# Optimization experiments

Measured on AMD Instinct MI355X. Metric: run time of the kernel, lower is better.

Reference implementation:

```python
import jax, jax.numpy as jnp
import numpy as np

GROUP_SIZE = 64

def _dequant(wq, scale, zero):
    # HQQ groupwise dequant: W = (Wq - zero) * scale, groups along input dim.
    out_dim, in_dim = wq.shape
    g = in_dim // GROUP_SIZE
    w = (wq.astype(jnp.float32).reshape(out_dim, g, GROUP_SIZE) - zero[:, :, None]) * scale[:, :, None]
    return w.reshape(out_dim, in_dim)

def setup_inputs() -> dict:
    key = jax.random.key(0)
    ks = jax.random.split(key, 10)
    T, H, I = 256, 4096, 14336
    G1, G2 = H // GROUP_SIZE, I // GROUP_SIZE  # 64, 224
    x = jax.random.normal(ks[0], (T, H), dtype=jnp.float32)
    w1_q = jax.random.randint(ks[1], (I, H), 0, 16, dtype=jnp.int32)
    w1_scale = jax.random.uniform(ks[2], (I, G1), dtype=jnp.float32) * 0.02
    w1_zero = jax.random.uniform(ks[3], (I, G1), dtype=jnp.float32) * 8.0
    w3_q = jax.random.randint(ks[4], (I, H), 0, 16, dtype=jnp.int32)
    w3_scale = jax.random.uniform(ks[5], (I, G1), dtype=jnp.float32) * 0.02
    w3_zero = jax.random.uniform(ks[6], (I, G1), dtype=jnp.float32) * 8.0
    w2_q = jax.random.randint(ks[7], (H, I), 0, 16, dtype=jnp.int32)
    w2_scale = jax.random.uniform(ks[8], (H, G2), dtype=jnp.float32) * 0.02
    w2_zero = jax.random.uniform(ks[9], (H, G2), dtype=jnp.float32) * 8.0
    return {"x": x, "w1_q": w1_q, "w1_scale": w1_scale, "w1_zero": w1_zero,
            "w3_q": w3_q, "w3_scale": w3_scale, "w3_zero": w3_zero,
            "w2_q": w2_q, "w2_scale": w2_scale, "w2_zero": w2_zero}

def reference(x, w1_q, w1_scale, w1_zero, w3_q, w3_scale, w3_zero, w2_q, w2_scale, w2_zero):
    w1 = _dequant(w1_q, w1_scale, w1_zero)  # [I, H]
    w3 = _dequant(w3_q, w3_scale, w3_zero)  # [I, H]
    w2 = _dequant(w2_q, w2_scale, w2_zero)  # [H, I]
    gate = jax.nn.silu(jnp.einsum('th,ih->ti', x, w1))  # [T, I]
    up = jnp.einsum('th,ih->ti', x, w3)                 # [T, I]
    return jnp.einsum('ti,hi->th', gate * up, w2)       # [T, H]
```

## Files before the change

kernel.cpp:

```cpp
#include <hip/hip_runtime.h>
#include <cstdint>
#include <cstddef>

#define T_DIM 256
#define H_DIM 4096
#define I_DIM 14336

typedef __attribute__((ext_vector_type(8))) short s8v;
typedef __attribute__((ext_vector_type(4))) float f4v;

static constexpr size_t XS_BYTES   = (size_t)T_DIM * H_DIM * 2;
static constexpr size_t ACT_OFF    = XS_BYTES;
static constexpr size_t ACT_BYTES  = (size_t)T_DIM * I_DIM * 2;
static constexpr size_t PART_OFF   = ACT_OFF + ACT_BYTES;
static constexpr size_t PART_BYTES = 8ull * T_DIM * H_DIM * 4;
static constexpr size_t WS_NEEDED  = PART_OFF + PART_BYTES;

__device__ __forceinline__ unsigned short f2bf(float f) {
    unsigned u = __builtin_bit_cast(unsigned, f);
    u += 0x7fffu + ((u >> 16) & 1u);
    return (unsigned short)(u >> 16);
}

__device__ __forceinline__ void bar_read() {
    __builtin_amdgcn_sched_barrier(0);
    __builtin_amdgcn_s_barrier();
    __builtin_amdgcn_sched_barrier(0);
}
__device__ __forceinline__ void bar_write() {
    __builtin_amdgcn_sched_barrier(0);
    asm volatile("s_waitcnt lgkmcnt(0)" ::: "memory");
    __builtin_amdgcn_s_barrier();
    __builtin_amdgcn_sched_barrier(0);
}

__device__ __forceinline__ s8v dq8(const int4 qa, const int4 qb, float s, float ns) {
    union { unsigned short u[8]; s8v v; } r;
    r.u[0] = f2bf(fmaf((float)qa.x, s, ns));
    r.u[1] = f2bf(fmaf((float)qa.y, s, ns));
    r.u[2] = f2bf(fmaf((float)qa.z, s, ns));
    r.u[3] = f2bf(fmaf((float)qa.w, s, ns));
    r.u[4] = f2bf(fmaf((float)qb.x, s, ns));
    r.u[5] = f2bf(fmaf((float)qb.y, s, ns));
    r.u[6] = f2bf(fmaf((float)qb.z, s, ns));
    r.u[7] = f2bf(fmaf((float)qb.w, s, ns));
    return r.v;
}

__global__ __launch_bounds__(256) void k_prep(const float* __restrict__ x,
                                              unsigned short* __restrict__ xs) {
    int gs   = blockIdx.x * 256 + threadIdx.x;
    int kt   = gs >> 11;
    int rem  = gs & 2047;
    int row  = rem >> 3;
    int slot = rem & 7;
    const float* xp = x + (size_t)row * H_DIM + kt * 64 + slot * 8;
    float4 a = *(const float4*)xp;
    float4 b = *(const float4*)(xp + 4);
    union { unsigned short u[8]; s8v v; } r;
    r.u[0] = f2bf(a.x); r.u[1] = f2bf(a.y); r.u[2] = f2bf(a.z); r.u[3] = f2bf(a.w);
    r.u[4] = f2bf(b.x); r.u[5] = f2bf(b.y); r.u[6] = f2bf(b.z); r.u[7] = f2bf(b.w);
    *(s8v*)(xs + (size_t)kt * 16384 + (size_t)row * 64 + (size_t)slot * 8) = r.v;
}

struct P1 { int4 x0, x1, x2, x3, q1a, q1b, q3a, q3b; float s1, z1, s3, z3; };

__global__ __launch_bounds__(512) void k_gemm1(
    const int* __restrict__ w1q, const float* __restrict__ w1s, const float* __restrict__ w1z,
    const int* __restrict__ w3q, const float* __restrict__ w3s, const float* __restrict__ w3z,
    const unsigned short* __restrict__ xs, unsigned short* __restrict__ act)
{
    __shared__ unsigned char lds[2][49152];
    const int tid  = threadIdx.x;
    const int blk  = blockIdx.x;
    const int n0   = blk * 64;
    const int wid  = tid >> 6;
    const int lane = tid & 63;
    const int wr   = wid >> 1;
    const int wc   = wid & 1;
    const int lr   = lane & 15;
    const int lkb  = lane >> 4;
    const int aswz = (lr & 7) << 4;

    const int sr = tid >> 3, sl = tid & 7;
    const int sbyte = sr * 128 + ((sl * 16) ^ ((sr & 7) << 4));
    const int4*  xbase = (const int4*)xs;
    const size_t wrow  = (size_t)(n0 + sr) * H_DIM;
    const float* s1p = w1s + (size_t)(n0 + sr) * 64;
    const float* z1p = w1z + (size_t)(n0 + sr) * 64;
    const float* s3p = w3s + (size_t)(n0 + sr) * 64;
    const float* z3p = w3z + (size_t)(n0 + sr) * 64;

    f4v accg[4][2], accu[4][2];
    const f4v fz = {0.f, 0.f, 0.f, 0.f};
    #pragma unroll
    for (int i = 0; i < 4; ++i)
        #pragma unroll
        for (int j = 0; j < 2; ++j) { accg[i][j] = fz; accu[i][j] = fz; }

    auto load = [&](int kt, P1& p) {
        const int4* xp = xbase + kt * 2048 + sr * 8 + sl;
        p.x0 = xp[0]; p.x1 = xp[512]; p.x2 = xp[1024]; p.x3 = xp[1536];
        const int4* p1 = (const int4*)(w1q + wrow + kt * 64 + sl * 8);
        const int4* p3 = (const int4*)(w3q + wrow + kt * 64 + sl * 8);
        p.q1a = p1[0]; p.q1b = p1[1]; p.q3a = p3[0]; p.q3b = p3[1];
        p.s1 = s1p[kt]; p.z1 = z1p[kt]; p.s3 = s3p[kt]; p.z3 = z3p[kt];
    };
    auto store = [&](const P1& p, unsigned char* b) {
        *(int4*)(b + sbyte)         = p.x0;
        *(int4*)(b + sbyte + 8192)  = p.x1;
        *(int4*)(b + sbyte + 16384) = p.x2;
        *(int4*)(b + sbyte + 24576) = p.x3;
        *(s8v*)(b + 32768 + sbyte) = dq8(p.q1a, p.q1b, p.s1, -p.z1 * p.s1);
        *(s8v*)(b + 40960 + sbyte) = dq8(p.q3a, p.q3b, p.s3, -p.z3 * p.s3);
    };
    auto compute = [&](const unsigned char* b) {
        #pragma unroll
        for (int kf = 0; kf < 2; ++kf) {
            const int kb = (kf * 64 + lkb * 16) ^ aswz;
            s8v a[4];
            #pragma unroll
            for (int mf = 0; mf < 4; ++mf)
                a[mf] = *(const s8v*)(b + (wr * 64 + mf * 16 + lr) * 128 + kb);
            s8v b1[2], b3[2];
            #pragma unroll
            for (int nf = 0; nf < 2; ++nf) {
                const int rbo = (wc * 32 + nf * 16 + lr) * 128 + kb;
                b1[nf] = *(const s8v*)(b + 32768 + rbo);
                b3[nf] = *(const s8v*)(b + 40960 + rbo);
            }
            #pragma unroll
            for (int mf = 0; mf < 4; ++mf)
                #pragma unroll
                for (int nf = 0; nf < 2; ++nf) {
                    accg[mf][nf] = __builtin_amdgcn_mfma_f32_16x16x32_bf16(a[mf], b1[nf], accg[mf][nf], 0, 0, 0);
                    accu[mf][nf] = __builtin_amdgcn_mfma_f32_16x16x32_bf16(a[mf], b3[nf], accu[mf][nf], 0, 0, 0);
                }
        }
    };

    P1 A, B;
    load(0, A);
    store(A, lds[0]);
    load(1, B);
    bar_write();

    for (int it = 0; it < 32; ++it) {
        const int t = it * 2;
        load(t + 2 > 63 ? 63 : t + 2, A);
        compute(lds[0]);
        bar_read();
        store(B, lds[1]);
        bar_write();
        load(t + 3 > 63 ? 63 : t + 3, B);
        compute(lds[1]);
        bar_read();
        store(A, lds[0]);
        bar_write();
    }

    unsigned char* actb = (unsigned char*)act + (size_t)blk * 32768;
    #pragma unroll
    for (int mf = 0; mf < 4; ++mf)
        #pragma unroll
        for (int nf = 0; nf < 2; ++nf)
            #pragma unroll
            for (int r = 0; r < 4; ++r) {
                const int m  = wr * 64 + mf * 16 + lkb * 4 + r;
                const int nl = wc * 32 + nf * 16 + lr;
                float g = accg[mf][nf][r];
                float u = accu[mf][nf][r];
                float sg = g / (1.0f + __expf(-g));
                *(unsigned short*)(actb + m * 128 + nl * 2) = f2bf(sg * u);
            }
}

struct P2 { int4 a0, a1, a2, a3, q0, q1, q2, q3; float s2, z2; };

template<bool ATOMIC>
__global__ __launch_bounds__(512) void k_gemm2(
    const int* __restrict__ w2q, const float* __restrict__ w2s, const float* __restrict__ w2z,
    const unsigned short* __restrict__ act, float* __restrict__ outp)
{
    __shared__ unsigned char lds[2][49152];
    const int tid  = threadIdx.x;
    const int nb   = blockIdx.x & 31;
    const int kc   = blockIdx.x >> 5;
    const int n0   = nb * 128;
    const int wid  = tid >> 6;
    const int lane = tid & 63;
    const int wr   = wid >> 2;
    const int wc   = wid & 3;
    const int lr   = lane & 15;
    const int lkb  = lane >> 4;
    const int aswz = (lr & 7) << 4;

    const int sr = tid >> 3, sl = tid & 7;
    const int abyte = sr * 128 + ((sl * 16) ^ ((sr & 7) << 4));
    const int r2 = tid >> 2, sq = tid & 3;
    const int wb0 = r2 * 128 + (((sq * 2) * 16)     ^ ((r2 & 7) << 4));
    const int wb1 = r2 * 128 + (((sq * 2 + 1) * 16) ^ ((r2 & 7) << 4));
    const int4*  abase = (const int4*)act;
    const size_t w2row = (size_t)(n0 + r2) * I_DIM;
    const float* s2p = w2s + (size_t)(n0 + r2) * 224;
    const float* z2p = w2z + (size_t)(n0 + r2) * 224;

    f4v acc[8][2];
    const f4v fz = {0.f, 0.f, 0.f, 0.f};
    #pragma unroll
    for (int i = 0; i < 8; ++i) { acc[i][0] = fz; acc[i][1] = fz; }

    auto load = [&](int kt, P2& p) {
        const int4* ap = abase + kt * 2048 + sr * 8 + sl;
        p.a0 = ap[0]; p.a1 = ap[512]; p.a2 = ap[1024]; p.a3 = ap[1536];
        const int4* wp = (const int4*)(w2q + w2row + kt * 64 + sq * 16);
        p.q0 = wp[0]; p.q1 = wp[1]; p.q2 = wp[2]; p.q3 = wp[3];
        p.s2 = s2p[kt]; p.z2 = z2p[kt];
    };
    auto store = [&](const P2& p, unsigned char* b) {
        *(int4*)(b + abyte)         = p.a0;
        *(int4*)(b + abyte + 8192)  = p.a1;
        *(int4*)(b + abyte + 16384) = p.a2;
        *(int4*)(b + abyte + 24576) = p.a3;
        float ns = -p.z2 * p.s2;
        *(s8v*)(b + 32768 + wb0) = dq8(p.q0, p.q1, p.s2, ns);
        *(s8v*)(b + 32768 + wb1) = dq8(p.q2, p.q3, p.s2, ns);
    };
    auto compute = [&](const unsigned char* b) {
        #pragma unroll
        for (int kf = 0; kf < 2; ++kf) {
            const int kb = (kf * 64 + lkb * 16) ^ aswz;
            s8v bfr[2];
            #pragma unroll
            for (int nf = 0; nf < 2; ++nf)
                bfr[nf] = *(const s8v*)(b + 32768 + (wc * 32 + nf * 16 + lr) * 128 + kb);
            #pragma unroll
            for (int mf = 0; mf < 8; ++mf) {
                s8v a = *(const s8v*)(b + (wr * 128 + mf * 16 + lr) * 128 + kb);
                acc[mf][0] = __builtin_amdgcn_mfma_f32_16x16x32_bf16(a, bfr[0], acc[mf][0], 0, 0, 0);
                acc[mf][1] = __builtin_amdgcn_mfma_f32_16x16x32_bf16(a, bfr[1], acc[mf][1], 0, 0, 0);
            }
        }
    };

    const int kt0 = kc * 28;
    P2 A, B;
    load(kt0, A);
    store(A, lds[0]);
    load(kt0 + 1, B);
    bar_write();

    for (int it = 0; it < 14; ++it) {
        const int t = it * 2;
        load(kt0 + (t + 2 > 27 ? 27 : t + 2), A);
        compute(lds[0]);
        bar_read();
        store(B, lds[1]);
        bar_write();
        load(kt0 + (t + 3 > 27 ? 27 : t + 3), B);
        compute(lds[1]);
        bar_read();
        store(A, lds[0]);
        bar_write();
    }

    float* pout = outp + (ATOMIC ? 0 : (size_t)kc * ((size_t)T_DIM * H_DIM));
    #pragma unroll
    for (int mf = 0; mf < 8; ++mf)
        #pragma unroll
        for (int nf = 0; nf < 2; ++nf)
            #pragma unroll
            for (int r = 0; r < 4; ++r) {
                const int m = wr * 128 + mf * 16 + lkb * 4 + r;
                const int n = n0 + wc * 32 + nf * 16 + lr;
                if (ATOMIC) atomicAdd(&outp[(size_t)m * H_DIM + n], acc[mf][nf][r]);
                else        pout[(size_t)m * H_DIM + n] = acc[mf][nf][r];
            }
}

__global__ __launch_bounds__(256) void k_reduce(const f4v* __restrict__ p,
                                                f4v* __restrict__ o) {
    int i = blockIdx.x * 256 + threadIdx.x;
    f4v s = p[i];
    #pragma unroll
    for (int c = 1; c < 8; ++c) s += p[(size_t)c * 262144 + i];
    o[i] = s;
}

__global__ __launch_bounds__(256) void k_zero(f4v* __restrict__ o) {
    o[blockIdx.x * 256 + threadIdx.x] = (f4v){0.f, 0.f, 0.f, 0.f};
}

extern "C" void kernel_launch(void* const* d_in, const int* in_sizes, int n_in,
                              void* d_out, int out_size, void* d_ws, size_t ws_size,
                              hipStream_t stream) {
    const float* x   = (const float*)d_in[0];
    const int*   w1q = (const int*)  d_in[1];
    const float* w1s = (const float*)d_in[2];
    const float* w1z = (const float*)d_in[3];
    const int*   w3q = (const int*)  d_in[4];
    const float* w3s = (const float*)d_in[5];
    const float* w3z = (const float*)d_in[6];
    const int*   w2q = (const int*)  d_in[7];
    const float* w2s = (const float*)d_in[8];
    const float* w2z = (const float*)d_in[9];
    float* outp = (float*)d_out;

    unsigned short* xs  = (unsigned short*)d_ws;
    unsigned short* act = (unsigned short*)((char*)d_ws + ACT_OFF);
    float*          prt = (float*)((char*)d_ws + PART_OFF);
    const bool partials = (ws_size >= WS_NEEDED);

    k_prep<<<512, 256, 0, stream>>>(x, xs);
    k_gemm1<<<224, 512, 0, stream>>>(w1q, w1s, w1z, w3q, w3s, w3z, xs, act);
    if (partials) {
        k_gemm2<false><<<256, 512, 0, stream>>>(w2q, w2s, w2z, act, prt);
        k_reduce<<<1024, 256, 0, stream>>>((const f4v*)prt, (f4v*)outp);
    } else {
        k_zero<<<1024, 256, 0, stream>>>((f4v*)outp);
        k_gemm2<true><<<256, 512, 0, stream>>>(w2q, w2s, w2z, act, outp);
    }
}
```

Measured before the change: 298.5 us.

## Shrink GEMM tiles, read activations directly from global, raise occupancy

Both GEMMs now use narrow 32-column weight tiles with only the dequantized weights staged in LDS. The activation operand (x in bf16, act) is read straight from global/L2 in row-major layout, and grid sizes double with launch bounds requesting 4 blocks per CU. The split-K for the second GEMM drops from 8 to 4 chunks, and both kernels use swizzled block ordering to improve L2 reuse. The aim is more occupancy and parallelism for the weight-bandwidth-bound dequant GEMMs, at the cost of far more redundant global/L2 reads of the activation matrices and less register-level reuse per MFMA.

```diff
diff --git a/kernel.cpp b/kernel.cpp
--- a/kernel.cpp
+++ b/kernel.cpp
@@ -7,13 +7,14 @@
 #define I_DIM 14336
 
 typedef __attribute__((ext_vector_type(8))) short s8v;
+typedef __attribute__((ext_vector_type(4))) short s4v;
 typedef __attribute__((ext_vector_type(4))) float f4v;
 
 static constexpr size_t XS_BYTES   = (size_t)T_DIM * H_DIM * 2;
 static constexpr size_t ACT_OFF    = XS_BYTES;
 static constexpr size_t ACT_BYTES  = (size_t)T_DIM * I_DIM * 2;
 static constexpr size_t PART_OFF   = ACT_OFF + ACT_BYTES;
-static constexpr size_t PART_BYTES = 8ull * T_DIM * H_DIM * 4;
+static constexpr size_t PART_BYTES = 4ull * T_DIM * H_DIM * 4;
 static constexpr size_t WS_NEEDED  = PART_OFF + PART_BYTES;
 
 __device__ __forceinline__ unsigned short f2bf(float f) {
@@ -34,103 +35,87 @@
     __builtin_amdgcn_sched_barrier(0);
 }
 
-__device__ __forceinline__ s8v dq8(const int4 qa, const int4 qb, float s, float ns) {
-    union { unsigned short u[8]; s8v v; } r;
-    r.u[0] = f2bf(fmaf((float)qa.x, s, ns));
-    r.u[1] = f2bf(fmaf((float)qa.y, s, ns));
-    r.u[2] = f2bf(fmaf((float)qa.z, s, ns));
-    r.u[3] = f2bf(fmaf((float)qa.w, s, ns));
-    r.u[4] = f2bf(fmaf((float)qb.x, s, ns));
-    r.u[5] = f2bf(fmaf((float)qb.y, s, ns));
-    r.u[6] = f2bf(fmaf((float)qb.z, s, ns));
-    r.u[7] = f2bf(fmaf((float)qb.w, s, ns));
+__device__ __forceinline__ s4v dq4(const int4 q, float s, float ns) {
+    union { unsigned short u[4]; s4v v; } r;
+    r.u[0] = f2bf(fmaf((float)q.x, s, ns));
+    r.u[1] = f2bf(fmaf((float)q.y, s, ns));
+    r.u[2] = f2bf(fmaf((float)q.z, s, ns));
+    r.u[3] = f2bf(fmaf((float)q.w, s, ns));
     return r.v;
 }
 
 __global__ __launch_bounds__(256) void k_prep(const float* __restrict__ x,
                                               unsigned short* __restrict__ xs) {
-    int gs   = blockIdx.x * 256 + threadIdx.x;
-    int kt   = gs >> 11;
-    int rem  = gs & 2047;
-    int row  = rem >> 3;
-    int slot = rem & 7;
-    const float* xp = x + (size_t)row * H_DIM + kt * 64 + slot * 8;
-    float4 a = *(const float4*)xp;
-    float4 b = *(const float4*)(xp + 4);
+    int i = (blockIdx.x * 256 + threadIdx.x) * 8;
+    float4 a = *(const float4*)(x + i);
+    float4 b = *(const float4*)(x + i + 4);
     union { unsigned short u[8]; s8v v; } r;
     r.u[0] = f2bf(a.x); r.u[1] = f2bf(a.y); r.u[2] = f2bf(a.z); r.u[3] = f2bf(a.w);
     r.u[4] = f2bf(b.x); r.u[5] = f2bf(b.y); r.u[6] = f2bf(b.z); r.u[7] = f2bf(b.w);
-    *(s8v*)(xs + (size_t)kt * 16384 + (size_t)row * 64 + (size_t)slot * 8) = r.v;
-}
-
-struct P1 { int4 x0, x1, x2, x3, q1a, q1b, q3a, q3b; float s1, z1, s3, z3; };
-
-__global__ __launch_bounds__(512) void k_gemm1(
+    *(s8v*)(xs + i) = r.v;
+}
+
+struct S1 { int4 q1, q3; float s1, z1, s3, z3; };
+
+__global__ __launch_bounds__(512, 4) void k_gemm1(
     const int* __restrict__ w1q, const float* __restrict__ w1s, const float* __restrict__ w1z,
     const int* __restrict__ w3q, const float* __restrict__ w3s, const float* __restrict__ w3z,
     const unsigned short* __restrict__ xs, unsigned short* __restrict__ act)
 {
-    __shared__ unsigned char lds[2][49152];
+    __shared__ unsigned char lds[2][8192];
     const int tid  = threadIdx.x;
-    const int blk  = blockIdx.x;
-    const int n0   = blk * 64;
+    const int swz  = (blockIdx.x & 7) * 56 + (blockIdx.x >> 3);
+    const int n0   = swz * 32;
     const int wid  = tid >> 6;
     const int lane = tid & 63;
-    const int wr   = wid >> 1;
-    const int wc   = wid & 1;
     const int lr   = lane & 15;
     const int lkb  = lane >> 4;
-    const int aswz = (lr & 7) << 4;
-
-    const int sr = tid >> 3, sl = tid & 7;
-    const int sbyte = sr * 128 + ((sl * 16) ^ ((sr & 7) << 4));
-    const int4*  xbase = (const int4*)xs;
-    const size_t wrow  = (size_t)(n0 + sr) * H_DIM;
-    const float* s1p = w1s + (size_t)(n0 + sr) * 64;
-    const float* z1p = w1z + (size_t)(n0 + sr) * 64;
-    const float* s3p = w3s + (size_t)(n0 + sr) * 64;
-    const float* z3p = w3z + (size_t)(n0 + sr) * 64;
-
-    f4v accg[4][2], accu[4][2];
+
+    const int row = tid >> 4, h = tid & 15;
+    const int4* w1p = (const int4*)w1q + (size_t)(n0 + row) * 1024;
+    const int4* w3p = (const int4*)w3q + (size_t)(n0 + row) * 1024;
+    const float* s1p = w1s + (size_t)(n0 + row) * 64;
+    const float* z1p = w1z + (size_t)(n0 + row) * 64;
+    const float* s3p = w3s + (size_t)(n0 + row) * 64;
+    const float* z3p = w3z + (size_t)(n0 + row) * 64;
+    const int wbyte = row * 128 + (((h >> 1) ^ (row & 7)) << 4) + ((h & 1) << 3);
+
+    const unsigned char* xsb = (const unsigned char*)xs;
+
+    f4v accg[2][2], accu[2][2];
     const f4v fz = {0.f, 0.f, 0.f, 0.f};
     #pragma unroll
-    for (int i = 0; i < 4; ++i)
+    for (int i = 0; i < 2; ++i)
         #pragma unroll
         for (int j = 0; j < 2; ++j) { accg[i][j] = fz; accu[i][j] = fz; }
 
-    auto load = [&](int kt, P1& p) {
-        const int4* xp = xbase + kt * 2048 + sr * 8 + sl;
-        p.x0 = xp[0]; p.x1 = xp[512]; p.x2 = xp[1024]; p.x3 = xp[1536];
-        const int4* p1 = (const int4*)(w1q + wrow + kt * 64 + sl * 8);
-        const int4* p3 = (const int4*)(w3q + wrow + kt * 64 + sl * 8);
-        p.q1a = p1[0]; p.q1b = p1[1]; p.q3a = p3[0]; p.q3b = p3[1];
-        p.s1 = s1p[kt]; p.z1 = z1p[kt]; p.s3 = s3p[kt]; p.z3 = z3p[kt];
-    };
-    auto store = [&](const P1& p, unsigned char* b) {
-        *(int4*)(b + sbyte)         = p.x0;
-        *(int4*)(b + sbyte + 8192)  = p.x1;
-        *(int4*)(b + sbyte + 16384) = p.x2;
-        *(int4*)(b + sbyte + 24576) = p.x3;
-        *(s8v*)(b + 32768 + sbyte) = dq8(p.q1a, p.q1b, p.s1, -p.z1 * p.s1);
-        *(s8v*)(b + 40960 + sbyte) = dq8(p.q3a, p.q3b, p.s3, -p.z3 * p.s3);
-    };
-    auto compute = [&](const unsigned char* b) {
+    auto load = [&](int kt, S1& p) {
+        p.q1 = w1p[kt * 16 + h];
+        p.q3 = w3p[kt * 16 + h];
+        p.s1 = s1p[kt]; p.z1 = z1p[kt];
+        p.s3 = s3p[kt]; p.z3 = z3p[kt];
+    };
+    auto store = [&](const S1& p, unsigned char* b) {
+        *(s4v*)(b + wbyte)        = dq4(p.q1, p.s1, -p.z1 * p.s1);
+        *(s4v*)(b + 4096 + wbyte) = dq4(p.q3, p.s3, -p.z3 * p.s3);
+    };
+    auto compute = [&](const unsigned char* b, int kt) {
         #pragma unroll
         for (int kf = 0; kf < 2; ++kf) {
-            const int kb = (kf * 64 + lkb * 16) ^ aswz;
-            s8v a[4];
-            #pragma unroll
-            for (int mf = 0; mf < 4; ++mf)
-                a[mf] = *(const s8v*)(b + (wr * 64 + mf * 16 + lr) * 128 + kb);
-            s8v b1[2], b3[2];
+            const int sw = kf * 4 + lkb;
+            s8v a[2], b1[2], b3[2];
             #pragma unroll
             for (int nf = 0; nf < 2; ++nf) {
-                const int rbo = (wc * 32 + nf * 16 + lr) * 128 + kb;
-                b1[nf] = *(const s8v*)(b + 32768 + rbo);
-                b3[nf] = *(const s8v*)(b + 40960 + rbo);
+                const int rbo = (nf * 16 + lr) * 128 + ((sw ^ (lr & 7)) << 4);
+                b1[nf] = *(const s8v*)(b + rbo);
+                b3[nf] = *(const s8v*)(b + 4096 + rbo);
             }
             #pragma unroll
-            for (int mf = 0; mf < 4; ++mf)
+            for (int mf = 0; mf < 2; ++mf)
+                a[mf] = *(const s8v*)(xsb + (size_t)(wid * 32 + mf * 16 + lr) * 8192
+                                          + kt * 128 + kf * 64 + lkb * 16);
+            #pragma unroll
+            for (int mf = 0; mf < 2; ++mf)
                 #pragma unroll
                 for (int nf = 0; nf < 2; ++nf) {
                     accg[mf][nf] = __builtin_amdgcn_mfma_f32_16x16x32_bf16(a[mf], b1[nf], accg[mf][nf], 0, 0, 0);
@@ -139,7 +124,7 @@
         }
     };
 
-    P1 A, B;
+    S1 A, B;
     load(0, A);
     store(A, lds[0]);
     load(1, B);
@@ -148,117 +133,107 @@
     for (int it = 0; it < 32; ++it) {
         const int t = it * 2;
         load(t + 2 > 63 ? 63 : t + 2, A);
-        compute(lds[0]);
+        compute(lds[0], t);
         bar_read();
         store(B, lds[1]);
         bar_write();
         load(t + 3 > 63 ? 63 : t + 3, B);
-        compute(lds[1]);
+        compute(lds[1], t + 1);
         bar_read();
         store(A, lds[0]);
         bar_write();
     }
 
-    unsigned char* actb = (unsigned char*)act + (size_t)blk * 32768;
-    #pragma unroll
-    for (int mf = 0; mf < 4; ++mf)
+    unsigned char* actb = (unsigned char*)act;
+    #pragma unroll
+    for (int mf = 0; mf < 2; ++mf)
         #pragma unroll
         for (int nf = 0; nf < 2; ++nf)
             #pragma unroll
             for (int r = 0; r < 4; ++r) {
-                const int m  = wr * 64 + mf * 16 + lkb * 4 + r;
-                const int nl = wc * 32 + nf * 16 + lr;
+                const int m = wid * 32 + mf * 16 + lkb * 4 + r;
+                const int n = n0 + nf * 16 + lr;
                 float g = accg[mf][nf][r];
                 float u = accu[mf][nf][r];
                 float sg = g / (1.0f + __expf(-g));
-                *(unsigned short*)(actb + m * 128 + nl * 2) = f2bf(sg * u);
+                *(unsigned short*)(actb + (size_t)m * (I_DIM * 2) + n * 2) = f2bf(sg * u);
             }
 }
 
-struct P2 { int4 a0, a1, a2, a3, q0, q1, q2, q3; float s2, z2; };
+struct S2 { int4 q2; float s2, z2; };
 
 template<bool ATOMIC>
-__global__ __launch_bounds__(512) void k_gemm2(
+__global__ __launch_bounds__(512, 4) void k_gemm2(
     const int* __restrict__ w2q, const float* __restrict__ w2s, const float* __restrict__ w2z,
     const unsigned short* __restrict__ act, float* __restrict__ outp)
 {
-    __shared__ unsigned char lds[2][49152];
+    __shared__ unsigned char lds[2][4096];
     const int tid  = threadIdx.x;
-    const int nb   = blockIdx.x & 31;
-    const int kc   = blockIdx.x >> 5;
-    const int n0   = nb * 128;
+    const int swz  = (blockIdx.x & 7) * 64 + (blockIdx.x >> 3);
+    const int kc   = swz >> 7;
+    const int nb   = swz & 127;
+    const int n0   = nb * 32;
     const int wid  = tid >> 6;
     const int lane = tid & 63;
-    const int wr   = wid >> 2;
-    const int wc   = wid & 3;
     const int lr   = lane & 15;
     const int lkb  = lane >> 4;
-    const int aswz = (lr & 7) << 4;
-
-    const int sr = tid >> 3, sl = tid & 7;
-    const int abyte = sr * 128 + ((sl * 16) ^ ((sr & 7) << 4));
-    const int r2 = tid >> 2, sq = tid & 3;
-    const int wb0 = r2 * 128 + (((sq * 2) * 16)     ^ ((r2 & 7) << 4));
-    const int wb1 = r2 * 128 + (((sq * 2 + 1) * 16) ^ ((r2 & 7) << 4));
-    const int4*  abase = (const int4*)act;
-    const size_t w2row = (size_t)(n0 + r2) * I_DIM;
-    const float* s2p = w2s + (size_t)(n0 + r2) * 224;
-    const float* z2p = w2z + (size_t)(n0 + r2) * 224;
-
-    f4v acc[8][2];
+
+    const int row = tid >> 4, h = tid & 15;
+    const int4* w2p = (const int4*)w2q + (size_t)(n0 + row) * 3584 + (size_t)kc * 896;
+    const float* s2p = w2s + (size_t)(n0 + row) * 224 + kc * 56;
+    const float* z2p = w2z + (size_t)(n0 + row) * 224 + kc * 56;
+    const int wbyte = row * 128 + (((h >> 1) ^ (row & 7)) << 4) + ((h & 1) << 3);
+
+    const unsigned char* actb = (const unsigned char*)act;
+    const size_t akc = (size_t)kc * 7168;
+
+    f4v acc[2][2];
     const f4v fz = {0.f, 0.f, 0.f, 0.f};
     #pragma unroll
-    for (int i = 0; i < 8; ++i) { acc[i][0] = fz; acc[i][1] = fz; }
-
-    auto load = [&](int kt, P2& p) {
-        const int4* ap = abase + kt * 2048 + sr * 8 + sl;
-        p.a0 = ap[0]; p.a1 = ap[512]; p.a2 = ap[1024]; p.a3 = ap[1536];
-        const int4* wp = (const int4*)(w2q + w2row + kt * 64 + sq * 16);
-        p.q0 = wp[0]; p.q1 = wp[1]; p.q2 = wp[2]; p.q3 = wp[3];
+    for (int i = 0; i < 2; ++i) { acc[i][0] = fz; acc[i][1] = fz; }
+
+    auto load = [&](int kt, S2& p) {
+        p.q2 = w2p[kt * 16 + h];
         p.s2 = s2p[kt]; p.z2 = z2p[kt];
     };
-    auto store = [&](const P2& p, unsigned char* b) {
-        *(int4*)(b + abyte)         = p.a0;
-        *(int4*)(b + abyte + 8192)  = p.a1;
-        *(int4*)(b + abyte + 16384) = p.a2;
-        *(int4*)(b + abyte + 24576) = p.a3;
-        float ns = -p.z2 * p.s2;
-        *(s8v*)(b + 32768 + wb0) = dq8(p.q0, p.q1, p.s2, ns);
-        *(s8v*)(b + 32768 + wb1) = dq8(p.q2, p.q3, p.s2, ns);
-    };
-    auto compute = [&](const unsigned char* b) {
+    auto store = [&](const S2& p, unsigned char* b) {
+        *(s4v*)(b + wbyte) = dq4(p.q2, p.s2, -p.z2 * p.s2);
+    };
+    auto compute = [&](const unsigned char* b, int kt) {
         #pragma unroll
         for (int kf = 0; kf < 2; ++kf) {
-            const int kb = (kf * 64 + lkb * 16) ^ aswz;
-            s8v bfr[2];
+            const int sw = kf * 4 + lkb;
+            s8v a[2], b2[2];
             #pragma unroll
             for (int nf = 0; nf < 2; ++nf)
-                bfr[nf] = *(const s8v*)(b + 32768 + (wc * 32 + nf * 16 + lr) * 128 + kb);
-            #pragma unroll
-            for (int mf = 0; mf < 8; ++mf) {
-                s8v a = *(const s8v*)(b + (wr * 128 + mf * 16 + lr) * 128 + kb);
-                acc[mf][0] = __builtin_amdgcn_mfma_f32_16x16x32_bf16(a, bfr[0], acc[mf][0], 0, 0, 0);
-                acc[mf][1] = __builtin_amdgcn_mfma_f32_16x16x32_bf16(a, bfr[1], acc[mf][1], 0, 0, 0);
-            }
+                b2[nf] = *(const s8v*)(b + (nf * 16 + lr) * 128 + ((sw ^ (lr & 7)) << 4));
+            #pragma unroll
+            for (int mf = 0; mf < 2; ++mf)
+                a[mf] = *(const s8v*)(actb + (size_t)(wid * 32 + mf * 16 + lr) * (I_DIM * 2)
+                                          + akc + kt * 128 + kf * 64 + lkb * 16);
+            #pragma unroll
+            for (int mf = 0; mf < 2; ++mf)
+                #pragma unroll
+                for (int nf = 0; nf < 2; ++nf)
+                    acc[mf][nf] = __builtin_amdgcn_mfma_f32_16x16x32_bf16(a[mf], b2[nf], acc[mf][nf], 0, 0, 0);
         }
     };
 
-    const int kt0 = kc * 28;
-    P2 A, B;
-    load(kt0, A);
+    S2 A, B;
+    load(0, A);
     store(A, lds[0]);
-    load(kt0 + 1, B);
+    load(1, B);
     bar_write();
 
-    for (int it = 0; it < 14; ++it) {
+    for (int it = 0; it < 28; ++it) {
         const int t = it * 2;
-        load(kt0 + (t + 2 > 27 ? 27 : t + 2), A);
-        compute(lds[0]);
+        load(t + 2 > 55 ? 55 : t + 2, A);
+        compute(lds[0], t);
         bar_read();
         store(B, lds[1]);
         bar_write();
-        load(kt0 + (t + 3 > 27 ? 27 : t + 3), B);
-        compute(lds[1]);
+        load(t + 3 > 55 ? 55 : t + 3, B);
+        compute(lds[1], t + 1);
         bar_read();
         store(A, lds[0]);
         bar_write();
@@ -266,13 +241,13 @@
 
     float* pout = outp + (ATOMIC ? 0 : (size_t)kc * ((size_t)T_DIM * H_DIM));
     #pragma unroll
-    for (int mf = 0; mf < 8; ++mf)
+    for (int mf = 0; mf < 2; ++mf)
         #pragma unroll
         for (int nf = 0; nf < 2; ++nf)
             #pragma unroll
             for (int r = 0; r < 4; ++r) {
-                const int m = wr * 128 + mf * 16 + lkb * 4 + r;
-                const int n = n0 + wc * 32 + nf * 16 + lr;
+                const int m = wid * 32 + mf * 16 + lkb * 4 + r;
+                const int n = n0 + nf * 16 + lr;
                 if (ATOMIC) atomicAdd(&outp[(size_t)m * H_DIM + n], acc[mf][nf][r]);
                 else        pout[(size_t)m * H_DIM + n] = acc[mf][nf][r];
             }
@@ -283,7 +258,7 @@
     int i = blockIdx.x * 256 + threadIdx.x;
     f4v s = p[i];
     #pragma unroll
-    for (int c = 1; c < 8; ++c) s += p[(size_t)c * 262144 + i];
+    for (int c = 1; c < 4; ++c) s += p[(size_t)c * 262144 + i];
     o[i] = s;
 }
 
@@ -312,12 +287,12 @@
     const bool partials = (ws_size >= WS_NEEDED);
 
     k_prep<<<512, 256, 0, stream>>>(x, xs);
-    k_gemm1<<<224, 512, 0, stream>>>(w1q, w1s, w1z, w3q, w3s, w3z, xs, act);
+    k_gemm1<<<448, 512, 0, stream>>>(w1q, w1s, w1z, w3q, w3s, w3z, xs, act);
     if (partials) {
-        k_gemm2<false><<<256, 512, 0, stream>>>(w2q, w2s, w2z, act, prt);
+        k_gemm2<false><<<512, 512, 0, stream>>>(w2q, w2s, w2z, act, prt);
         k_reduce<<<1024, 256, 0, stream>>>((const f4v*)prt, (f4v*)outp);
     } else {
         k_zero<<<1024, 256, 0, stream>>>((f4v*)outp);
-        k_gemm2<true><<<256, 512, 0, stream>>>(w2q, w2s, w2z, act, outp);
+        k_gemm2<true><<<512, 512, 0, stream>>>(w2q, w2s, w2z, act, outp);
     }
 }
```

New measurement: 334.9 us. 12.2% more time.
